# Performance work log

Measured on AMD Instinct MI355X. Metric: run time of the kernel, lower is better.

Reference implementation:

```python
import math
import jax, jax.numpy as jnp
import numpy as np

B, S, E = 4, 2048, 768
H, D = 12, 64
LOCAL_H, GLOBAL_H = 8, 4
WINDOW_BASE, MIN_W, MAX_W = 128, 32, 512
GLOBAL_RATIO = 0.1
MASK_VALUE = -1e9


def setup_inputs() -> dict:
    key = jax.random.key(0)
    k1, k2, k3 = jax.random.split(key, 3)
    return {
        "x": jax.random.normal(k1, (B, S, E), dtype=jnp.float32),
        "w_attn": jax.random.normal(k2, (E, 3 * E), dtype=jnp.float32) * 0.02,
        "b_attn": jnp.zeros((3 * E,), dtype=jnp.float32),
        "w_proj": jax.random.normal(k3, (E, E), dtype=jnp.float32) * 0.02,
        "b_proj": jnp.zeros((E,), dtype=jnp.float32),
    }


def _masks(seq_len: int):
    # dynamic window (adaptive): base * sqrt(S/base), clamped
    w = int(WINDOW_BASE * math.sqrt(seq_len / WINDOW_BASE))
    w = max(MIN_W, min(w, MAX_W))
    half = w // 2
    i = jnp.arange(seq_len)[:, None]
    j = jnp.arange(seq_len)[None, :]
    # local: window band then causal override -> allowed iff i-half <= j <= i
    local_allowed = (j >= i - half) & (j <= i)
    local_mask = jnp.where(local_allowed, 0.0, MASK_VALUE).astype(jnp.float32)
    # global: columns at linspace positions allowed for all rows, plus full causal
    n_glob = max(1, int(seq_len * GLOBAL_RATIO))
    gpos = jnp.linspace(0.0, seq_len - 1, n_glob).astype(jnp.int32)
    is_gcol = jnp.zeros((seq_len,), dtype=bool).at[gpos].set(True)
    global_allowed = (j <= i) | is_gcol[None, :]
    global_mask = jnp.where(global_allowed, 0.0, MASK_VALUE).astype(jnp.float32)
    return local_mask, global_mask


def _attend(q, k, v, mask):
    # q,k,v: [B,h,S,D]; mask: [S,S]
    scale = 1.0 / math.sqrt(q.shape[-1])
    scores = jnp.einsum("bhqd,bhkd->bhqk", q, k) * scale + mask[None, None]
    w = jax.nn.softmax(scores, axis=-1)
    return jnp.einsum("bhqk,bhkd->bhqd", w, v)


def reference(x, w_attn, b_attn, w_proj, b_proj):
    b, s, _ = x.shape
    qkv = x @ w_attn + b_attn                       # [B,S,3E]
    q, k, v = jnp.split(qkv, 3, axis=-1)
    def heads(t):
        return t.reshape(b, s, H, D).transpose(0, 2, 1, 3)  # [B,H,S,D]
    q, k, v = heads(q), heads(k), heads(v)
    local_mask, global_mask = _masks(s)
    local_out = _attend(q[:, :LOCAL_H], k[:, :LOCAL_H], v[:, :LOCAL_H], local_mask)
    global_out = _attend(q[:, LOCAL_H:], k[:, LOCAL_H:], v[:, LOCAL_H:], global_mask)
    attn = jnp.concatenate([local_out, global_out], axis=1)  # heads 0..7 local, 8..11 global
    attn = attn.transpose(0, 2, 1, 3).reshape(b, s, E)
    return attn @ w_proj + b_proj
```

## Files before the change

### kernel.cpp

```cpp
#include <hip/hip_runtime.h>
#include <stdint.h>


#define NH 12
#define SQ 2048

typedef __bf16 bf16x8 __attribute__((ext_vector_type(8)));
typedef float f32x4 __attribute__((ext_vector_type(4)));

#define GLOAD_LDS16(g, l)                                                      \
  __builtin_amdgcn_global_load_lds(                                            \
      (__attribute__((address_space(1))) void*)(g),                            \
      (__attribute__((address_space(3))) void*)(l), 16, 0, 0)

__device__ __forceinline__ unsigned short bfbits(float f) {
  __bf16 h = (__bf16)f;
  return *(unsigned short*)&h;
}

__global__ __launch_bounds__(256) void prep(
    const float* __restrict__ x, unsigned short* __restrict__ xb,
    const float* __restrict__ w_attn, unsigned short* __restrict__ wattnT,
    const float* __restrict__ w_proj, unsigned short* __restrict__ wprojT) {
  const int bid = blockIdx.x, t = threadIdx.x;
  if (bid < 512) {
    const int n4 = 8192 * 768 / 4;
    for (int i = bid * 256 + t; i < n4; i += 512 * 256) {
      float4 v = ((const float4*)x)[i];
      ((ushort4*)xb)[i] = make_ushort4(bfbits(v.x), bfbits(v.y), bfbits(v.z), bfbits(v.w));
    }
    return;
  }
  __shared__ float tile[32][33];
  const float* in; unsigned short* out; int K, N, tl;
  if (bid < 512 + 72 * 24) { in = w_attn; out = wattnT; K = 768; N = 2304; tl = bid - 512; }
  else                     { in = w_proj; out = wprojT; K = 768; N = 768;  tl = bid - 512 - 72 * 24; }
  const int tpr = N / 32;
  const int n0 = (tl % tpr) * 32, k0 = (tl / tpr) * 32;
  const int tx = t & 31, ty = t >> 5;
  for (int r = ty; r < 32; r += 8) tile[r][tx] = in[(size_t)(k0 + r) * N + n0 + tx];
  __syncthreads();
  for (int r = ty; r < 32; r += 8) out[(size_t)(n0 + r) * K + k0 + tx] = bfbits(tile[tx][r]);
}

__global__ __launch_bounds__(256) void vprep(const unsigned short* __restrict__ QKV,
                                             unsigned short* __restrict__ Vtb,
                                             unsigned short* __restrict__ Kg,
                                             unsigned short* __restrict__ VgT,
                                             int* __restrict__ gidx) {
  const int id = blockIdx.x, t = threadIdx.x;
  if (id < 1536) {
    const int bh = id >> 5, b = bh / NH, h = bh % NH;
    const int s0 = (id & 31) * 64;
    __shared__ unsigned short T[64][72];
    const int r = t >> 2, c0 = (t & 3) * 16;
    const size_t src = (size_t)(b * SQ + s0 + r) * 2304 + 1536 + h * 64 + c0;
    *(uint4*)&T[r][c0]     = *(const uint4*)&QKV[src];
    *(uint4*)&T[r][c0 + 8] = *(const uint4*)&QKV[src + 8];
    __syncthreads();
    unsigned short pk[16];
#pragma unroll
    for (int z = 0; z < 16; ++z) pk[z] = T[c0 + z][r];
    size_t dst = (size_t)bh * 131072 + (size_t)r * 2048 + s0 + c0;
    *(uint4*)&Vtb[dst]     = *(uint4*)&pk[0];
    *(uint4*)&Vtb[dst + 8] = *(uint4*)&pk[8];
    return;
  }
  const int g = id - 1536;
  const int bh = g >> 3, y = g & 7;
  const int b = bh >> 2, h = 8 + (bh & 3);
  if (g == 0) {
    int c = t;
    gidx[c] = (c < 203) ? (int)((double)c * (2047.0 / 203.0)) : ((c == 203) ? 2047 : -1);
  }
  {
    int c = t, ch = y;
    int col = (c < 203) ? (int)((double)c * (2047.0 / 203.0)) : ((c == 203) ? 2047 : -1);
    uint4 v = {0u, 0u, 0u, 0u};
    if (col >= 0) v = *(const uint4*)&QKV[(size_t)(b * SQ + col) * 2304 + 768 + h * 64 + ch * 8];
    *(uint4*)&Kg[((size_t)bh * 256 + c) * 64 + ch * 8] = v;
  }
  {
    int d = t >> 2;
    int cb = (t & 3) * 64 + y * 8;
    for (int cc = 0; cc < 8; ++cc) {
      int c = cb + cc;
      int col = (c < 203) ? (int)((double)c * (2047.0 / 203.0)) : ((c == 203) ? 2047 : -1);
      unsigned short v = 0;
      if (col >= 0) v = QKV[(size_t)(b * SQ + col) * 2304 + 1536 + h * 64 + d];
      VgT[((size_t)bh * 64 + d) * 256 + c] = v;
    }
  }
}

__device__ __forceinline__ void gemm_mainloop(
    const unsigned short* __restrict__ A, const unsigned short* __restrict__ BT,
    int m0, int n0, int tid,
    unsigned short* As, unsigned short* Bs,
    f32x4 acc[4][4]) {
  const int lane = tid & 63, wave = tid >> 6;
  const int wm = wave >> 1, wn = wave & 1;
  const int ln = lane & 15, quad = lane >> 4;
  const int arow = wave * 16 + (lane >> 2);
  const int acol = (lane & 3) * 8;

#pragma unroll
  for (int mi = 0; mi < 4; ++mi)
#pragma unroll
    for (int ni = 0; ni < 4; ++ni) acc[mi][ni] = (f32x4){0.f, 0.f, 0.f, 0.f};

  for (int kt = 0; kt < 12; ++kt) {
    const int k0 = kt * 64;
    __syncthreads();
#pragma unroll
    for (int p = 0; p < 2; ++p) {
      const int ldso = (p * 64 + wave * 16) * 32;
      GLOAD_LDS16(A  + (size_t)(m0 + p * 64 + arow) * 768 + k0 + acol,       &As[ldso]);
      GLOAD_LDS16(A  + (size_t)(m0 + p * 64 + arow) * 768 + k0 + 32 + acol,  &As[4096 + ldso]);
      GLOAD_LDS16(BT + (size_t)(n0 + p * 64 + arow) * 768 + k0 + acol,       &Bs[ldso]);
      GLOAD_LDS16(BT + (size_t)(n0 + p * 64 + arow) * 768 + k0 + 32 + acol,  &Bs[4096 + ldso]);
    }
    __syncthreads();
#pragma unroll
    for (int kh = 0; kh < 2; ++kh) {
      const int base = kh * 4096;
      bf16x8 aF[4], bF[4];
#pragma unroll
      for (int mi = 0; mi < 4; ++mi)
        aF[mi] = *(const bf16x8*)&As[base + (wm * 64 + mi * 16 + ln) * 32 + quad * 8];
#pragma unroll
      for (int ni = 0; ni < 4; ++ni)
        bF[ni] = *(const bf16x8*)&Bs[base + (wn * 64 + ni * 16 + ln) * 32 + quad * 8];
#pragma unroll
      for (int mi = 0; mi < 4; ++mi)
#pragma unroll
        for (int ni = 0; ni < 4; ++ni)
          acc[mi][ni] = __builtin_amdgcn_mfma_f32_16x16x32_bf16(aF[mi], bF[ni], acc[mi][ni], 0, 0, 0);
    }
  }
}

__global__ __launch_bounds__(256) void qkv_gemm(
    const unsigned short* __restrict__ Xb, const unsigned short* __restrict__ WT,
    const float* __restrict__ bias, unsigned short* __restrict__ Out) {
  __shared__ __attribute__((aligned(16))) unsigned short As[2 * 128 * 32];
  __shared__ __attribute__((aligned(16))) unsigned short Bs[2 * 128 * 32];
  f32x4 acc[4][4];
  const int m0 = blockIdx.y * 128, n0 = blockIdx.x * 128;
  const int tid = threadIdx.x;
  gemm_mainloop(Xb, WT, m0, n0, tid, As, Bs, acc);
  const int lane = tid & 63, wave = tid >> 6;
  const int wm = wave >> 1, wn = wave & 1, ln = lane & 15, quad = lane >> 4;
#pragma unroll
  for (int mi = 0; mi < 4; ++mi)
#pragma unroll
    for (int ni = 0; ni < 4; ++ni) {
      int n = n0 + wn * 64 + ni * 16 + ln;
      float bs = bias[n];
#pragma unroll
      for (int rg = 0; rg < 4; ++rg) {
        int m = m0 + wm * 64 + mi * 16 + quad * 4 + rg;
        Out[(size_t)m * 2304 + n] = bfbits(acc[mi][ni][rg] + bs);
      }
    }
}

__global__ __launch_bounds__(256) void proj_gemm(
    const unsigned short* __restrict__ Ab, const unsigned short* __restrict__ WT,
    const float* __restrict__ bias, float* __restrict__ Out) {
  __shared__ __attribute__((aligned(16))) unsigned short As[2 * 128 * 32];
  __shared__ __attribute__((aligned(16))) unsigned short Bs[2 * 128 * 32];
  f32x4 acc[4][4];
  const int m0 = blockIdx.y * 128, n0 = blockIdx.x * 128;
  const int tid = threadIdx.x;
  gemm_mainloop(Ab, WT, m0, n0, tid, As, Bs, acc);
  const int lane = tid & 63, wave = tid >> 6;
  const int wm = wave >> 1, wn = wave & 1, ln = lane & 15, quad = lane >> 4;
#pragma unroll
  for (int mi = 0; mi < 4; ++mi)
#pragma unroll
    for (int ni = 0; ni < 4; ++ni)
#pragma unroll
      for (int rg = 0; rg < 4; ++rg) {
        int m = m0 + wm * 64 + mi * 16 + quad * 4 + rg;
        int n = n0 + wn * 64 + ni * 16 + ln;
        Out[(size_t)m * 768 + n] = acc[mi][ni][rg] + bias[n];
      }
}

__global__ __launch_bounds__(256, 5) void attn_kernel(
    const unsigned short* __restrict__ QKV,
    const unsigned short* __restrict__ Vtb,
    const unsigned short* __restrict__ Kg, const unsigned short* __restrict__ VgT,
    const int* __restrict__ gidx,
    unsigned short* __restrict__ AOut,
    unsigned short* __restrict__ Opart,
    float* __restrict__ Lpart) {
  __shared__ __attribute__((aligned(16))) unsigned short Ks[64 * 72];
  __shared__ __attribute__((aligned(16))) unsigned short Vs[64 * 72];
  __shared__ __attribute__((aligned(16))) unsigned short Ps[64 * 72];

  const int gid = blockIdx.x;
  int b, h, qb, vt0, vt1;
  bool multi = false;
  if (gid < 1536) {
    int bh = gid / 96, rem = gid % 96;
    b = bh >> 2; h = 8 + (bh & 3);
    int part;
    if (rem < 4)       { qb = rem;                               part = 0; }
    else if (rem < 20) { int z = rem - 4;  qb = 4 + (z >> 1);    part = z & 1; }
    else if (rem < 44) { int z = rem - 20; int q = z / 3; qb = 12 + q; part = z - 3 * q; }
    else if (rem < 76) { int z = rem - 44; qb = 20 + (z >> 2);   part = z & 3; }
    else               { int z = rem - 76; int q = z / 5; qb = 28 + q; part = z - 5 * q; }
    vt0 = part * 8;
    vt1 = min(vt0 + 8, qb + 5);
    multi = (qb >= 4);
  } else {
    int lid = gid - 1536;
    int bh = lid >> 5; b = bh >> 3; h = bh & 7; qb = lid & 31;
    vt0 = ((qb > 4) ? qb - 4 : 0) + 4;
    vt1 = qb + 5;
  }
  const int qb0 = qb * 64;
  const bool is_local = (h < 8);
  const int tid = threadIdx.x, lane = tid & 63, wave = tid >> 6;
  const int ln = lane & 15, quad = lane >> 4;
  const int bh48 = b * NH + h;
  const int bhg = (b << 2) | (h & 3);

  const size_t qoff = (size_t)(b * SQ + qb0 + wave * 16 + ln) * 2304 + h * 64;
  bf16x8 qA0 = *(const bf16x8*)&QKV[qoff + quad * 8];
  bf16x8 qA1 = *(const bf16x8*)&QKV[qoff + 32 + quad * 8];

  bf16x8 onesF;
#pragma unroll
  for (int z = 0; z < 8; ++z) onesF[z] = (__bf16)1.0f;

  f32x4 o[4];
  f32x4 ls = (f32x4){0.f, 0.f, 0.f, 0.f};
#pragma unroll
  for (int dt = 0; dt < 4; ++dt) o[dt] = (f32x4){0.f, 0.f, 0.f, 0.f};

  const int irow = qb0 + wave * 16 + quad * 4;
  const int iw = qb0 + wave * 16;
  const int sr = tid >> 3, sch = tid & 7;

  uint4 pk0, pk1, pv0, pv1;
  auto issue_load = [&](int vt) {
    if (vt >= 4) {
      const int kstart = (vt - 4) * 64;
      const size_t ko = (size_t)(b * SQ + kstart + sr) * 2304 + 768 + h * 64 + sch * 8;
      pk0 = *(const uint4*)&QKV[ko];
      pk1 = *(const uint4*)&QKV[ko + (size_t)32 * 2304];
      const size_t vo = (size_t)bh48 * 131072 + (size_t)sr * 2048 + kstart + sch * 8;
      pv0 = *(const uint4*)&Vtb[vo];
      pv1 = *(const uint4*)&Vtb[vo + 32 * 2048];
    } else {
      const int kg0 = vt * 64;
      pk0 = *(const uint4*)&Kg[((size_t)bhg * 256 + kg0 + sr) * 64 + sch * 8];
      pk1 = *(const uint4*)&Kg[((size_t)bhg * 256 + kg0 + 32 + sr) * 64 + sch * 8];
      pv0 = *(const uint4*)&VgT[((size_t)bhg * 64 + sr) * 256 + kg0 + sch * 8];
      pv1 = *(const uint4*)&VgT[((size_t)bhg * 64 + 32 + sr) * 256 + kg0 + sch * 8];
    }
  };
  issue_load(vt0);

  for (int vt = vt0; vt < vt1; ++vt) {
    const bool gph = (vt < 4);
    __syncthreads();
    *(uint4*)&Ks[sr * 72 + sch * 8]        = pk0;
    *(uint4*)&Ks[(32 + sr) * 72 + sch * 8] = pk1;
    *(uint4*)&Vs[sr * 72 + sch * 8]        = pv0;
    *(uint4*)&Vs[(32 + sr) * 72 + sch * 8] = pv1;
    __syncthreads();
    if (vt + 1 < vt1) issue_load(vt + 1);

    const int kstart = (vt - 4) * 64;
    const int kg0 = vt * 64;
    float sc[4][4];
    const bool full = !gph && (kstart + 63 <= iw) && (!is_local || kstart >= iw - 241);
#pragma unroll
    for (int nt = 0; nt < 4; ++nt) {
      bf16x8 kF0 = *(const bf16x8*)&Ks[(nt * 16 + ln) * 72 + quad * 8];
      bf16x8 kF1 = *(const bf16x8*)&Ks[(nt * 16 + ln) * 72 + 32 + quad * 8];
      f32x4 c = (f32x4){0.f, 0.f, 0.f, 0.f};
      c = __builtin_amdgcn_mfma_f32_16x16x32_bf16(qA0, kF0, c, 0, 0, 0);
      c = __builtin_amdgcn_mfma_f32_16x16x32_bf16(qA1, kF1, c, 0, 0, 0);
      if (full) {
#pragma unroll
        for (int rg = 0; rg < 4; ++rg) sc[nt][rg] = c[rg] * 0.125f - 8.f;
      } else if (!gph) {
        int j = kstart + nt * 16 + ln;
#pragma unroll
        for (int rg = 0; rg < 4; ++rg) {
          int i = irow + rg;
          bool ok = is_local ? (j >= i - 256 && j <= i) : (j <= i);
          sc[nt][rg] = ok ? (c[rg] * 0.125f - 8.f) : -1e9f;
        }
      } else {
        int jg = gidx[kg0 + nt * 16 + ln];
#pragma unroll
        for (int rg = 0; rg < 4; ++rg) {
          bool ok = jg > (irow + rg);
          sc[nt][rg] = ok ? (c[rg] * 0.125f - 8.f) : -1e9f;
        }
      }
    }

    __bf16* P = (__bf16*)Ps;
#pragma unroll
    for (int rg = 0; rg < 4; ++rg) {
      int prow = (wave * 16 + quad * 4 + rg) * 72;
#pragma unroll
      for (int nt = 0; nt < 4; ++nt)
        P[prow + nt * 16 + ln] = (__bf16)__expf(sc[nt][rg]);
    }
    bf16x8 pF0 = *(const bf16x8*)&Ps[(wave * 16 + ln) * 72 + quad * 8];
    bf16x8 pF1 = *(const bf16x8*)&Ps[(wave * 16 + ln) * 72 + 32 + quad * 8];
    ls = __builtin_amdgcn_mfma_f32_16x16x32_bf16(pF0, onesF, ls, 0, 0, 0);
    ls = __builtin_amdgcn_mfma_f32_16x16x32_bf16(pF1, onesF, ls, 0, 0, 0);
#pragma unroll
    for (int dt = 0; dt < 4; ++dt) {
      bf16x8 vF0 = *(const bf16x8*)&Vs[(dt * 16 + ln) * 72 + quad * 8];
      bf16x8 vF1 = *(const bf16x8*)&Vs[(dt * 16 + ln) * 72 + 32 + quad * 8];
      o[dt] = __builtin_amdgcn_mfma_f32_16x16x32_bf16(pF0, vF0, o[dt], 0, 0, 0);
      o[dt] = __builtin_amdgcn_mfma_f32_16x16x32_bf16(pF1, vF1, o[dt], 0, 0, 0);
    }
  }

  if (gid >= 1536 || !multi) {
#pragma unroll
    for (int dt = 0; dt < 4; ++dt)
#pragma unroll
      for (int rg = 0; rg < 4; ++rg) {
        int row = b * SQ + qb0 + wave * 16 + quad * 4 + rg;
        int e = h * 64 + dt * 16 + ln;
        AOut[(size_t)row * 768 + e] = bfbits(o[dt][rg] / ls[rg]);
      }
  } else {
#pragma unroll
    for (int dt = 0; dt < 4; ++dt)
#pragma unroll
      for (int rg = 0; rg < 4; ++rg) {
        int row = wave * 16 + quad * 4 + rg;
        Opart[(size_t)gid * 4096 + row * 64 + dt * 16 + ln] = bfbits(o[dt][rg]);
      }
    if (ln == 0) {
#pragma unroll
      for (int rg = 0; rg < 4; ++rg)
        Lpart[(size_t)gid * 64 + wave * 16 + quad * 4 + rg] = ls[rg];
    }
  }
}

__global__ __launch_bounds__(256) void combine_parts(
    const unsigned short* __restrict__ Opart, const float* __restrict__ Lpart,
    unsigned short* __restrict__ AOut) {
  const int bid = blockIdx.x;
  const int bh = bid / 28, qb = bid % 28 + 4;
  const int b = bh >> 2, h = 8 + (bh & 3);
  int C, np;
  if (qb < 12)      { C = 2 * qb - 4;  np = 2; }
  else if (qb < 20) { C = 3 * qb - 16; np = 3; }
  else if (qb < 28) { C = 4 * qb - 36; np = 4; }
  else              { C = 5 * qb - 64; np = 5; }
  const int slot0 = bh * 96 + C;
  const int t = threadIdx.x, r = t >> 2, c0 = (t & 3) * 16;
  float acc[16];
#pragma unroll
  for (int z = 0; z < 16; ++z) acc[z] = 0.f;
  float l = 0.f;
  for (int p = 0; p < np; ++p) {
    const unsigned short* src = &Opart[(size_t)(slot0 + p) * 4096 + r * 64 + c0];
    bf16x8 v0 = *(const bf16x8*)&src[0];
    bf16x8 v1 = *(const bf16x8*)&src[8];
#pragma unroll
    for (int z = 0; z < 8; ++z) { acc[z] += (float)v0[z]; acc[8 + z] += (float)v1[z]; }
    l += Lpart[(size_t)(slot0 + p) * 64 + r];
  }
  float inv = 1.f / l;
  unsigned short pk[16];
#pragma unroll
  for (int z = 0; z < 16; ++z) pk[z] = bfbits(acc[z] * inv);
  size_t dst = (size_t)(b * SQ + qb * 64 + r) * 768 + h * 64 + c0;
  *(uint4*)&AOut[dst]     = *(uint4*)&pk[0];
  *(uint4*)&AOut[dst + 8] = *(uint4*)&pk[8];
}

extern "C" void kernel_launch(void* const* d_in, const int* in_sizes, int n_in,
                              void* d_out, int out_size, void* d_ws, size_t ws_size,
                              hipStream_t stream) {
  const float* x      = (const float*)d_in[0];
  const float* w_attn = (const float*)d_in[1];
  const float* b_attn = (const float*)d_in[2];
  const float* w_proj = (const float*)d_in[3];
  const float* b_proj = (const float*)d_in[4];
  float* out = (float*)d_out;

  char* ws = (char*)d_ws;
  size_t off = 0;
  auto alloc = [&](size_t bytes) {
    void* p = ws + off;
    off += (bytes + 255) & ~(size_t)255;
    return p;
  };
  unsigned short* xb     = (unsigned short*)alloc((size_t)8192 * 768 * 2);
  unsigned short* wattnT = (unsigned short*)alloc((size_t)2304 * 768 * 2);
  unsigned short* wprojT = (unsigned short*)alloc((size_t)768 * 768 * 2);
  unsigned short* qkvb   = (unsigned short*)alloc((size_t)8192 * 2304 * 2);
  unsigned short* Vtb    = (unsigned short*)alloc((size_t)48 * 64 * 2048 * 2);
  unsigned short* Kgb    = (unsigned short*)alloc((size_t)16 * 256 * 64 * 2);
  unsigned short* VgTb   = (unsigned short*)alloc((size_t)16 * 64 * 256 * 2);
  int* gidxb             = (int*)alloc((size_t)256 * 4);
  unsigned short* Opartb = (unsigned short*)alloc((size_t)1536 * 4096 * 2);
  float* Lpartb          = (float*)alloc((size_t)1536 * 64 * 4);
  unsigned short* attnb  = xb;

  prep<<<dim3(512 + 72 * 24 + 24 * 24), dim3(256), 0, stream>>>(
      x, xb, w_attn, wattnT, w_proj, wprojT);
  qkv_gemm<<<dim3(18, 64), dim3(256), 0, stream>>>(xb, wattnT, b_attn, qkvb);
  vprep<<<dim3(1536 + 128), dim3(256), 0, stream>>>(qkvb, Vtb, Kgb, VgTb, gidxb);
  attn_kernel<<<dim3(2560), dim3(256), 0, stream>>>(qkvb, Vtb, Kgb, VgTb, gidxb,
                                                    attnb, Opartb, Lpartb);
  combine_parts<<<dim3(448), dim3(256), 0, stream>>>(Opartb, Lpartb, attnb);
  proj_gemm<<<dim3(6, 64), dim3(256), 0, stream>>>(attnb, wprojT, b_proj, out);
}
```

Measured before the change: 211.6 us.

## Swizzle attention LDS tiles, use exp2, remap GEMM block order for XCDs

```diff
diff --git a/kernel.cpp b/kernel.cpp
--- a/kernel.cpp
+++ b/kernel.cpp
@@ -146,7 +146,8 @@
   __shared__ __attribute__((aligned(16))) unsigned short As[2 * 128 * 32];
   __shared__ __attribute__((aligned(16))) unsigned short Bs[2 * 128 * 32];
   f32x4 acc[4][4];
-  const int m0 = blockIdx.y * 128, n0 = blockIdx.x * 128;
+  const int wg = (blockIdx.x & 7) * 144 + (blockIdx.x >> 3);
+  const int m0 = (wg / 18) * 128, n0 = (wg % 18) * 128;
   const int tid = threadIdx.x;
   gemm_mainloop(Xb, WT, m0, n0, tid, As, Bs, acc);
   const int lane = tid & 63, wave = tid >> 6;
@@ -171,7 +172,8 @@
   __shared__ __attribute__((aligned(16))) unsigned short As[2 * 128 * 32];
   __shared__ __attribute__((aligned(16))) unsigned short Bs[2 * 128 * 32];
   f32x4 acc[4][4];
-  const int m0 = blockIdx.y * 128, n0 = blockIdx.x * 128;
+  const int wg = (blockIdx.x & 7) * 48 + (blockIdx.x >> 3);
+  const int m0 = (wg / 6) * 128, n0 = (wg % 6) * 128;
   const int tid = threadIdx.x;
   gemm_mainloop(Ab, WT, m0, n0, tid, As, Bs, acc);
   const int lane = tid & 63, wave = tid >> 6;
@@ -188,7 +190,7 @@
       }
 }
 
-__global__ __launch_bounds__(256, 5) void attn_kernel(
+__global__ __launch_bounds__(256, 6) void attn_kernel(
     const unsigned short* __restrict__ QKV,
     const unsigned short* __restrict__ Vtb,
     const unsigned short* __restrict__ Kg, const unsigned short* __restrict__ VgT,
@@ -196,9 +198,9 @@
     unsigned short* __restrict__ AOut,
     unsigned short* __restrict__ Opart,
     float* __restrict__ Lpart) {
-  __shared__ __attribute__((aligned(16))) unsigned short Ks[64 * 72];
-  __shared__ __attribute__((aligned(16))) unsigned short Vs[64 * 72];
-  __shared__ __attribute__((aligned(16))) unsigned short Ps[64 * 72];
+  __shared__ __attribute__((aligned(16))) unsigned short Ks[64 * 64];
+  __shared__ __attribute__((aligned(16))) unsigned short Vs[64 * 64];
+  __shared__ __attribute__((aligned(16))) unsigned short Ps[64 * 64];
 
   const int gid = blockIdx.x;
   int b, h, qb, vt0, vt1;
@@ -244,6 +246,12 @@
   const int irow = qb0 + wave * 16 + quad * 4;
   const int iw = qb0 + wave * 16;
   const int sr = tid >> 3, sch = tid & 7;
+  const int ssw = (sch ^ (sr & 7)) * 8;
+  const int s0k = (quad ^ (ln & 7)) * 8;
+  const int s1k = ((quad + 4) ^ (ln & 7)) * 8;
+  const int lnh = ln >> 3, ln7 = ln & 7;
+
+  const float S2 = 0.125f * 1.44269504f, B2 = 8.0f * 1.44269504f;
 
   uint4 pk0, pk1, pv0, pv1;
   auto issue_load = [&](int vt) {
@@ -268,10 +276,10 @@
   for (int vt = vt0; vt < vt1; ++vt) {
     const bool gph = (vt < 4);
     __syncthreads();
-    *(uint4*)&Ks[sr * 72 + sch * 8]        = pk0;
-    *(uint4*)&Ks[(32 + sr) * 72 + sch * 8] = pk1;
-    *(uint4*)&Vs[sr * 72 + sch * 8]        = pv0;
-    *(uint4*)&Vs[(32 + sr) * 72 + sch * 8] = pv1;
+    *(uint4*)&Ks[sr * 64 + ssw]        = pk0;
+    *(uint4*)&Ks[(32 + sr) * 64 + ssw] = pk1;
+    *(uint4*)&Vs[sr * 64 + ssw]        = pv0;
+    *(uint4*)&Vs[(32 + sr) * 64 + ssw] = pv1;
     __syncthreads();
     if (vt + 1 < vt1) issue_load(vt + 1);
 
@@ -281,28 +289,28 @@
     const bool full = !gph && (kstart + 63 <= iw) && (!is_local || kstart >= iw - 241);
 #pragma unroll
     for (int nt = 0; nt < 4; ++nt) {
-      bf16x8 kF0 = *(const bf16x8*)&Ks[(nt * 16 + ln) * 72 + quad * 8];
-      bf16x8 kF1 = *(const bf16x8*)&Ks[(nt * 16 + ln) * 72 + 32 + quad * 8];
+      bf16x8 kF0 = *(const bf16x8*)&Ks[(nt * 16 + ln) * 64 + s0k];
+      bf16x8 kF1 = *(const bf16x8*)&Ks[(nt * 16 + ln) * 64 + s1k];
       f32x4 c = (f32x4){0.f, 0.f, 0.f, 0.f};
       c = __builtin_amdgcn_mfma_f32_16x16x32_bf16(qA0, kF0, c, 0, 0, 0);
       c = __builtin_amdgcn_mfma_f32_16x16x32_bf16(qA1, kF1, c, 0, 0, 0);
       if (full) {
 #pragma unroll
-        for (int rg = 0; rg < 4; ++rg) sc[nt][rg] = c[rg] * 0.125f - 8.f;
+        for (int rg = 0; rg < 4; ++rg) sc[nt][rg] = c[rg] * S2 - B2;
       } else if (!gph) {
         int j = kstart + nt * 16 + ln;
 #pragma unroll
         for (int rg = 0; rg < 4; ++rg) {
           int i = irow + rg;
           bool ok = is_local ? (j >= i - 256 && j <= i) : (j <= i);
-          sc[nt][rg] = ok ? (c[rg] * 0.125f - 8.f) : -1e9f;
+          sc[nt][rg] = ok ? (c[rg] * S2 - B2) : -1e9f;
         }
       } else {
         int jg = gidx[kg0 + nt * 16 + ln];
 #pragma unroll
         for (int rg = 0; rg < 4; ++rg) {
           bool ok = jg > (irow + rg);
-          sc[nt][rg] = ok ? (c[rg] * 0.125f - 8.f) : -1e9f;
+          sc[nt][rg] = ok ? (c[rg] * S2 - B2) : -1e9f;
         }
       }
     }
@@ -310,19 +318,21 @@
     __bf16* P = (__bf16*)Ps;
 #pragma unroll
     for (int rg = 0; rg < 4; ++rg) {
-      int prow = (wave * 16 + quad * 4 + rg) * 72;
+      int prow = wave * 16 + quad * 4 + rg;
+      int pbase = prow * 64 + ln7;
+      int pr7 = prow & 7;
 #pragma unroll
       for (int nt = 0; nt < 4; ++nt)
-        P[prow + nt * 16 + ln] = (__bf16)__expf(sc[nt][rg]);
-    }
-    bf16x8 pF0 = *(const bf16x8*)&Ps[(wave * 16 + ln) * 72 + quad * 8];
-    bf16x8 pF1 = *(const bf16x8*)&Ps[(wave * 16 + ln) * 72 + 32 + quad * 8];
+        P[pbase + (((nt * 2 + lnh) ^ pr7) << 3)] = (__bf16)exp2f(sc[nt][rg]);
+    }
+    bf16x8 pF0 = *(const bf16x8*)&Ps[(wave * 16 + ln) * 64 + s0k];
+    bf16x8 pF1 = *(const bf16x8*)&Ps[(wave * 16 + ln) * 64 + s1k];
     ls = __builtin_amdgcn_mfma_f32_16x16x32_bf16(pF0, onesF, ls, 0, 0, 0);
     ls = __builtin_amdgcn_mfma_f32_16x16x32_bf16(pF1, onesF, ls, 0, 0, 0);
 #pragma unroll
     for (int dt = 0; dt < 4; ++dt) {
-      bf16x8 vF0 = *(const bf16x8*)&Vs[(dt * 16 + ln) * 72 + quad * 8];
-      bf16x8 vF1 = *(const bf16x8*)&Vs[(dt * 16 + ln) * 72 + 32 + quad * 8];
+      bf16x8 vF0 = *(const bf16x8*)&Vs[(dt * 16 + ln) * 64 + s0k];
+      bf16x8 vF1 = *(const bf16x8*)&Vs[(dt * 16 + ln) * 64 + s1k];
       o[dt] = __builtin_amdgcn_mfma_f32_16x16x32_bf16(pF0, vF0, o[dt], 0, 0, 0);
       o[dt] = __builtin_amdgcn_mfma_f32_16x16x32_bf16(pF1, vF1, o[dt], 0, 0, 0);
     }
@@ -418,10 +428,10 @@
 
   prep<<<dim3(512 + 72 * 24 + 24 * 24), dim3(256), 0, stream>>>(
       x, xb, w_attn, wattnT, w_proj, wprojT);
-  qkv_gemm<<<dim3(18, 64), dim3(256), 0, stream>>>(xb, wattnT, b_attn, qkvb);
+  qkv_gemm<<<dim3(1152), dim3(256), 0, stream>>>(xb, wattnT, b_attn, qkvb);
   vprep<<<dim3(1536 + 128), dim3(256), 0, stream>>>(qkvb, Vtb, Kgb, VgTb, gidxb);
   attn_kernel<<<dim3(2560), dim3(256), 0, stream>>>(qkvb, Vtb, Kgb, VgTb, gidxb,
                                                     attnb, Opartb, Lpartb);
   combine_parts<<<dim3(448), dim3(256), 0, stream>>>(Opartb, Lpartb, attnb);
-  proj_gemm<<<dim3(6, 64), dim3(256), 0, stream>>>(attnb, wprojT, b_proj, out);
-}
+  proj_gemm<<<dim3(384), dim3(256), 0, stream>>>(attnb, wprojT, b_proj, out);
+}
```

Result: slower. 297.4 us (+40.6%).
